# Optimization experiments

Measured on AMD Instinct MI355X. Metric: run time of the kernel, lower is better.

## Reference

```python
import jax, jax.numpy as jnp
import numpy as np

N_NODES = 50000
N_EDGES = 1_600_000
D_FEAT = 128


def setup_inputs() -> dict:
    key = jax.random.key(0)
    k1, k2, k3 = jax.random.split(key, 3)
    x = jax.random.normal(k1, (N_NODES, D_FEAT), dtype=jnp.float32)
    # Valid CSR rowptr: sorted, rowptr[0] = 0, rowptr[-1] = N_EDGES.
    inner = jnp.sort(jax.random.randint(k2, (N_NODES - 1,), 0, N_EDGES + 1))
    rowptr = jnp.concatenate([
        jnp.zeros((1,), jnp.int64) if False else jnp.array([0], dtype=jnp.int32),
        inner.astype(jnp.int32),
        jnp.array([N_EDGES], dtype=jnp.int32),
    ]).astype(jnp.int64)
    col = jax.random.randint(k3, (N_EDGES,), 0, N_NODES).astype(jnp.int64)
    return {"x": x, "rowptr": rowptr, "col": col}


def reference(x, rowptr, col):
    """CSR SpMM with sum aggregation: out[i] = sum_{j in [rowptr[i], rowptr[i+1])} x[col[j]]."""
    n_nodes = rowptr.shape[0] - 1
    n_edges = col.shape[0]
    # Recover row id of each edge from rowptr (jit-friendly, no dynamic repeat).
    row = jnp.searchsorted(rowptr, jnp.arange(n_edges, dtype=rowptr.dtype), side="right") - 1
    gathered = x[col]  # [E, D]
    out = jax.ops.segment_sum(gathered, row, num_segments=n_nodes)  # [N, D]
    return out
```

## Files before the change

### kernel.cpp

```cpp
#include <hip/hip_runtime.h>


typedef float f32x4 __attribute__((ext_vector_type(4)));
typedef unsigned int u32;

__global__ __launch_bounds__(256) void cvt_bf16_kernel(
    const float2* __restrict__ x2, u32* __restrict__ xb, int npairs)
{
    for (int i = blockIdx.x * 256 + threadIdx.x; i < npairs; i += gridDim.x * 256) {
        const float2 f = x2[i];
        u32 a = __float_as_uint(f.x);
        a = (a + 0x7FFFu + ((a >> 16) & 1u)) >> 16;
        u32 b = __float_as_uint(f.y);
        b = (b + 0x7FFFu + ((b >> 16) & 1u)) & 0xFFFF0000u;
        xb[i] = a | b;
    }
}

__device__ __forceinline__ void addv(float* acc, const uint4 v) {
    acc[0] += __uint_as_float(v.x << 16);
    acc[1] += __uint_as_float(v.x & 0xFFFF0000u);
    acc[2] += __uint_as_float(v.y << 16);
    acc[3] += __uint_as_float(v.y & 0xFFFF0000u);
    acc[4] += __uint_as_float(v.z << 16);
    acc[5] += __uint_as_float(v.z & 0xFFFF0000u);
    acc[6] += __uint_as_float(v.w << 16);
    acc[7] += __uint_as_float(v.w & 0xFFFF0000u);
}

__global__ __launch_bounds__(256) void spmm_bf16_kernel(
    const uint4* __restrict__ xb,
    const int*   __restrict__ rowptr,
    const int*   __restrict__ col,
    float*       __restrict__ out,
    int n_nodes)
{
    const int lane16 = threadIdx.x & 15;
    const int grp    = threadIdx.x >> 4;
    const int row    = blockIdx.x * 16 + grp;
    if (row >= n_nodes) return;

    const uint4* xbl = xb + lane16;
    const int r1 = rowptr[row + 1];
    int j = rowptr[row];

    float acc[8] = {0.f, 0.f, 0.f, 0.f, 0.f, 0.f, 0.f, 0.f};

    for (; j + 8 <= r1; j += 8) {
        const int c0 = col[j + 0];
        const int c1 = col[j + 1];
        const int c2 = col[j + 2];
        const int c3 = col[j + 3];
        const int c4 = col[j + 4];
        const int c5 = col[j + 5];
        const int c6 = col[j + 6];
        const int c7 = col[j + 7];
        const uint4 v0 = xbl[(size_t)c0 * 16];
        const uint4 v1 = xbl[(size_t)c1 * 16];
        const uint4 v2 = xbl[(size_t)c2 * 16];
        const uint4 v3 = xbl[(size_t)c3 * 16];
        const uint4 v4 = xbl[(size_t)c4 * 16];
        const uint4 v5 = xbl[(size_t)c5 * 16];
        const uint4 v6 = xbl[(size_t)c6 * 16];
        const uint4 v7 = xbl[(size_t)c7 * 16];
        addv(acc, v0); addv(acc, v1); addv(acc, v2); addv(acc, v3);
        addv(acc, v4); addv(acc, v5); addv(acc, v6); addv(acc, v7);
    }
    for (; j < r1; ++j) {
        const uint4 v = xbl[(size_t)col[j] * 16];
        addv(acc, v);
    }

    float* dst = out + (size_t)row * 128 + lane16 * 8;
    ((f32x4*)dst)[0] = (f32x4){acc[0], acc[1], acc[2], acc[3]};
    ((f32x4*)dst)[1] = (f32x4){acc[4], acc[5], acc[6], acc[7]};
}

__global__ __launch_bounds__(256) void spmm_f32_kernel(
    const f32x4* __restrict__ x4,
    const int*   __restrict__ rowptr,
    const int*   __restrict__ col,
    f32x4*       __restrict__ out4,
    int n_nodes)
{
    const int lane = threadIdx.x & 31;
    const int grp  = threadIdx.x >> 5;
    const int row  = blockIdx.x * 8 + grp;
    if (row >= n_nodes) return;

    const int r1 = rowptr[row + 1];
    int j = rowptr[row];
    f32x4 acc = {0.f, 0.f, 0.f, 0.f};
    for (; j + 4 <= r1; j += 4) {
        const int c0 = col[j + 0];
        const int c1 = col[j + 1];
        const int c2 = col[j + 2];
        const int c3 = col[j + 3];
        f32x4 a = x4[(size_t)c0 * 32 + lane];
        f32x4 b = x4[(size_t)c1 * 32 + lane];
        f32x4 c = x4[(size_t)c2 * 32 + lane];
        f32x4 d = x4[(size_t)c3 * 32 + lane];
        acc += a; acc += b; acc += c; acc += d;
    }
    for (; j < r1; ++j) acc += x4[(size_t)col[j] * 32 + lane];
    out4[(size_t)row * 32 + lane] = acc;
}

extern "C" void kernel_launch(void* const* d_in, const int* in_sizes, int n_in,
                              void* d_out, int out_size, void* d_ws, size_t ws_size,
                              hipStream_t stream) {
    const float* x      = (const float*)d_in[0];
    const int*   rowptr = (const int*)d_in[1];
    const int*   col    = (const int*)d_in[2];
    float*       out    = (float*)d_out;

    const int n_nodes = in_sizes[1] - 1;
    const int n_feats = in_sizes[0] / (in_sizes[1] - 1);
    const size_t xb_bytes = (size_t)in_sizes[0] * 2;

    if (ws_size >= xb_bytes && n_feats == 128) {
        u32* xb = (u32*)d_ws;
        const int npairs = in_sizes[0] / 2;
        cvt_bf16_kernel<<<2048, 256, 0, stream>>>((const float2*)x, xb, npairs);
        const int blocks = (n_nodes + 15) / 16;
        spmm_bf16_kernel<<<blocks, 256, 0, stream>>>(
            (const uint4*)xb, rowptr, col, out, n_nodes);
    } else {
        const int blocks = (n_nodes + 7) / 8;
        spmm_f32_kernel<<<blocks, 256, 0, stream>>>(
            (const f32x4*)x, rowptr, col, (f32x4*)out, n_nodes);
    }
}
```

Baseline: 80.77 us.

## Assign one wavefront per row with four sub-groups splitting edges

The bf16 SpMM kernel now maps one 64-lane wavefront to each row instead of one 16-lane group. Four 16-lane sub-groups take interleaved edges and combine their partial sums with xor shuffles before one sub-group writes the row. This splits each row's edge list across more lanes so more gathers are in flight per row and long rows finish sooner, at the cost of shuffle reductions and four times as many blocks. Column-index loads and output stores now use nontemporal hints.

After: 66.77 us (median of 2 runs). -17.3%, faster.

```diff
diff --git a/kernel.cpp b/kernel.cpp
--- a/kernel.cpp
+++ b/kernel.cpp
@@ -28,52 +28,58 @@
     acc[7] += __uint_as_float(v.w & 0xFFFF0000u);
 }
 
-__global__ __launch_bounds__(256) void spmm_bf16_kernel(
+__global__ __launch_bounds__(256) void spmm_rowwave_kernel(
     const uint4* __restrict__ xb,
     const int*   __restrict__ rowptr,
     const int*   __restrict__ col,
     float*       __restrict__ out,
     int n_nodes)
 {
-    const int lane16 = threadIdx.x & 15;
-    const int grp    = threadIdx.x >> 4;
-    const int row    = blockIdx.x * 16 + grp;
+    const int wave = threadIdx.x >> 6;
+    const int lane = threadIdx.x & 63;
+    const int sub  = lane >> 4;
+    const int l16  = lane & 15;
+    const int row  = blockIdx.x * 4 + wave;
     if (row >= n_nodes) return;
 
-    const uint4* xbl = xb + lane16;
+    const uint4* xbl = xb + l16;
+    const int r0 = rowptr[row];
     const int r1 = rowptr[row + 1];
-    int j = rowptr[row];
 
     float acc[8] = {0.f, 0.f, 0.f, 0.f, 0.f, 0.f, 0.f, 0.f};
 
-    for (; j + 8 <= r1; j += 8) {
-        const int c0 = col[j + 0];
-        const int c1 = col[j + 1];
-        const int c2 = col[j + 2];
-        const int c3 = col[j + 3];
-        const int c4 = col[j + 4];
-        const int c5 = col[j + 5];
-        const int c6 = col[j + 6];
-        const int c7 = col[j + 7];
+    int j = r0;
+    for (; j + 16 <= r1; j += 16) {
+        const int c0 = __builtin_nontemporal_load(col + j + sub + 0);
+        const int c1 = __builtin_nontemporal_load(col + j + sub + 4);
+        const int c2 = __builtin_nontemporal_load(col + j + sub + 8);
+        const int c3 = __builtin_nontemporal_load(col + j + sub + 12);
         const uint4 v0 = xbl[(size_t)c0 * 16];
         const uint4 v1 = xbl[(size_t)c1 * 16];
         const uint4 v2 = xbl[(size_t)c2 * 16];
         const uint4 v3 = xbl[(size_t)c3 * 16];
-        const uint4 v4 = xbl[(size_t)c4 * 16];
-        const uint4 v5 = xbl[(size_t)c5 * 16];
-        const uint4 v6 = xbl[(size_t)c6 * 16];
-        const uint4 v7 = xbl[(size_t)c7 * 16];
         addv(acc, v0); addv(acc, v1); addv(acc, v2); addv(acc, v3);
-        addv(acc, v4); addv(acc, v5); addv(acc, v6); addv(acc, v7);
     }
-    for (; j < r1; ++j) {
-        const uint4 v = xbl[(size_t)col[j] * 16];
-        addv(acc, v);
+    for (; j + 4 <= r1; j += 4) {
+        const int c = __builtin_nontemporal_load(col + j + sub);
+        addv(acc, xbl[(size_t)c * 16]);
+    }
+    if (j + sub < r1) {
+        const int c = __builtin_nontemporal_load(col + j + sub);
+        addv(acc, xbl[(size_t)c * 16]);
     }
 
-    float* dst = out + (size_t)row * 128 + lane16 * 8;
-    ((f32x4*)dst)[0] = (f32x4){acc[0], acc[1], acc[2], acc[3]};
-    ((f32x4*)dst)[1] = (f32x4){acc[4], acc[5], acc[6], acc[7]};
+    #pragma unroll
+    for (int k = 0; k < 8; ++k) {
+        acc[k] += __shfl_xor(acc[k], 16, 64);
+        acc[k] += __shfl_xor(acc[k], 32, 64);
+    }
+
+    if (sub == 0) {
+        float* dst = out + (size_t)row * 128 + l16 * 8;
+        __builtin_nontemporal_store((f32x4){acc[0], acc[1], acc[2], acc[3]}, (f32x4*)dst);
+        __builtin_nontemporal_store((f32x4){acc[4], acc[5], acc[6], acc[7]}, (f32x4*)(dst + 4));
+    }
 }
 
 __global__ __launch_bounds__(256) void spmm_f32_kernel(
@@ -115,15 +121,15 @@
     float*       out    = (float*)d_out;
 
     const int n_nodes = in_sizes[1] - 1;
-    const int n_feats = in_sizes[0] / (in_sizes[1] - 1);
+    const int n_feats = (n_nodes > 0) ? in_sizes[0] / n_nodes : 0;
     const size_t xb_bytes = (size_t)in_sizes[0] * 2;
 
     if (ws_size >= xb_bytes && n_feats == 128) {
         u32* xb = (u32*)d_ws;
         const int npairs = in_sizes[0] / 2;
         cvt_bf16_kernel<<<2048, 256, 0, stream>>>((const float2*)x, xb, npairs);
-        const int blocks = (n_nodes + 15) / 16;
-        spmm_bf16_kernel<<<blocks, 256, 0, stream>>>(
+        const int blocks = (n_nodes + 3) / 4;
+        spmm_rowwave_kernel<<<blocks, 256, 0, stream>>>(
             (const uint4*)xb, rowptr, col, out, n_nodes);
     } else {
         const int blocks = (n_nodes + 7) / 8;
```
